# Kernel tuning notes

Measured on AMD Instinct MI355X. Metric: run time of the kernel, lower is better.

The kernel has to match this reference:

```python
import jax, jax.numpy as jnp
from jax import lax
import numpy as np

HEADS = 4
FACTOR = 4
EPS = 1e-12  # torch F.normalize eps


def _to_heads(t):
    # b (head c) (h1 fy) (w1 fx) -> b head (c fx fy) (h1 w1)
    b, C, h, w = t.shape
    c = C // HEADS
    h1, w1 = h // FACTOR, w // FACTOR
    t = t.reshape(b, HEADS, c, h1, FACTOR, w1, FACTOR)       # b,head,c,h1,fy,w1,fx
    t = t.transpose(0, 1, 2, 6, 4, 3, 5)                      # b,head,c,fx,fy,h1,w1
    return t.reshape(b, HEADS, c * FACTOR * FACTOR, h1 * w1)


def _from_heads(t, h, w):
    # b head (c fx fy) (h1 w1) -> b (head c) (h1 fy) (w1 fx)
    b = t.shape[0]
    c = t.shape[2] // (FACTOR * FACTOR)
    h1, w1 = h // FACTOR, w // FACTOR
    t = t.reshape(b, HEADS, c, FACTOR, FACTOR, h1, w1)        # b,head,c,fx,fy,h1,w1
    t = t.transpose(0, 1, 2, 5, 4, 6, 3)                      # b,head,c,h1,fy,w1,fx
    return t.reshape(b, HEADS * c, h, w)


def _l2norm(t):
    n = jnp.sqrt(jnp.sum(t * t, axis=-1, keepdims=True))
    return t / jnp.maximum(n, EPS)


def setup_inputs() -> dict:
    key = jax.random.key(0)
    ks = jax.random.split(key, 4)
    dim = 192
    x = jax.random.normal(ks[0], (8, dim, 128, 128), jnp.float32)
    qkv_w = jax.random.normal(ks[1], (3 * dim, dim), jnp.float32) * 0.05
    qkv_b = jnp.zeros((3 * dim,), jnp.float32)
    dw_w = jax.random.normal(ks[2], (3 * dim, 1, 3, 3), jnp.float32) * 0.05
    dw_b = jnp.zeros((3 * dim,), jnp.float32)
    proj_w = jax.random.normal(ks[3], (dim, dim), jnp.float32) * 0.05
    proj_b = jnp.zeros((dim,), jnp.float32)
    temperature = jnp.ones((HEADS, 1, 1), jnp.float32)
    return dict(x=x, qkv_w=qkv_w, qkv_b=qkv_b, dw_w=dw_w, dw_b=dw_b,
                proj_w=proj_w, proj_b=proj_b, temperature=temperature)


def reference(x, qkv_w, qkv_b, dw_w, dw_b, proj_w, proj_b, temperature):
    b, c, h, w = x.shape
    # 1x1 conv qkv
    qkv = jnp.einsum('bchw,oc->bohw', x, qkv_w) + qkv_b[None, :, None, None]
    # 3x3 depthwise conv (groups = 3*dim)
    qkv = lax.conv_general_dilated(
        qkv, dw_w, window_strides=(1, 1), padding=((1, 1), (1, 1)),
        feature_group_count=3 * c,
        dimension_numbers=('NCHW', 'OIHW', 'NCHW')) + dw_b[None, :, None, None]
    q, k, v = jnp.split(qkv, 3, axis=1)
    # H,W are multiples of FACTOR so the module's pad/unpad is a no-op
    q = _l2norm(_to_heads(q))
    k = _l2norm(_to_heads(k))
    v = _to_heads(v)
    # channel-wise attention: [b,head,d,d] with d = (c/head)*16
    attn = jnp.einsum('bhdn,bhen->bhde', q, k) * temperature[None]
    # softmax_1: exp(x) / (sum exp(x) + 1)
    e = jnp.exp(attn)
    attn = e / (jnp.sum(e, axis=-1, keepdims=True) + 1.0)
    out = jnp.einsum('bhde,bhen->bhdn', attn, v)
    out = _from_heads(out, h, w)
    out = jnp.einsum('bchw,oc->bohw', out, proj_w) + proj_b[None, :, None, None]
    return out
```

## Files before the change

### kernel.cpp

```cpp
#include <hip/hip_runtime.h>

#define HW 16384
#define CDIM 192

typedef short bf16x8 __attribute__((ext_vector_type(8)));
typedef short short8 __attribute__((ext_vector_type(8)));
typedef short short4_t __attribute__((ext_vector_type(4)));
typedef float f32x4  __attribute__((ext_vector_type(4)));

__device__ inline void gload_lds16(const void* g, void* l) {
  __builtin_amdgcn_global_load_lds(
      (const __attribute__((address_space(1))) void*)g,
      (__attribute__((address_space(3))) void*)l, 16, 0, 0);
}

__device__ inline short to_bf16_rne(float f) {
  unsigned u = __float_as_uint(f);
  unsigned r = u + 0x7fffu + ((u >> 16) & 1u);
  return (short)(r >> 16);
}

__device__ inline float b2f(short s) {
  return __uint_as_float(((unsigned)(unsigned short)s) << 16);
}

__device__ inline void split_bf16(float a, short& hi, short& lo) {
  unsigned u = __float_as_uint(a);
  hi = (short)(u >> 16);
  float res = a - __uint_as_float(u & 0xffff0000u);
  lo = (short)(__float_as_uint(res) >> 16);
}

__global__ __launch_bounds__(256) void k_zero(float* __restrict__ p, int n) {
  int i = blockIdx.x * 256 + threadIdx.x;
  if (i < n) p[i] = 0.f;
}

__global__ __launch_bounds__(256) void k_split_w(
    const float* __restrict__ W, short* __restrict__ hi,
    short* __restrict__ lo, int n)
{
  int i = blockIdx.x * 256 + threadIdx.x;
  if (i < n) { short h, l; split_bf16(W[i], h, l); hi[i] = h; lo[i] = l; }
}

#define CMM_LOADB(bv, k0)                                                     \
  { _Pragma("unroll")                                                         \
    for (int kk = 0; kk < 2; ++kk) {                                          \
      const int kcg = kg0 + kk * 2;                                           \
      _Pragma("unroll")                                                       \
      for (int j = 0; j < 8; ++j)                                             \
        bv[kk][j] = xf[(size_t)((k0) + kcg * 8 + j) * HW + n0 + px];          \
    } }

#define CMM_STAGEA1(k0, b)                                                    \
  { _Pragma("unroll")                                                         \
    for (int ii = 0; ii < 3; ++ii) {                                          \
      const int mf = w * 3 + ii;                                   \
      const short* g = Whi + (size_t)(m0 + mf * 16 + lr) * CDIM + (k0) + lq * 8; \
      gload_lds16(g, Ah[b] + mf * 512);                                       \
    } }

#define CMM_WRITEB1(bv, b)                                                    \
  { _Pragma("unroll")                                                         \
    for (int kk = 0; kk < 2; ++kk) {                                          \
      const int kcg = kg0 + kk * 2;                                           \
      short8 s8;                                                              \
      _Pragma("unroll")                                                       \
      for (int j = 0; j < 8; ++j) s8[j] = to_bf16_rne(bv[kk][j]);             \
      *(short8*)&Bh[b][(kcg * 128 + px) * 8] = s8;                            \
    } }

#define CMM_STAGE_PROJ(k0, b)                                                 \
  { _Pragma("unroll")                                                         \
    for (int ii = 0; ii < 6; ++ii) {                                          \
      const int id = w * 6 + ii, arr = id / 12, mf = id % 12;                 \
      const short* Wp = arr ? Wlo : Whi;                                      \
      const short* g = Wp + (size_t)(m0 + mf * 16 + lr) * CDIM + (k0) + lq * 8; \
      gload_lds16(g, (arr ? Al[b] : Ah[b]) + mf * 512);                       \
    }                                                                         \
    _Pragma("unroll")                                                         \
    for (int ii = 0; ii < 4; ++ii) {                                          \
      const int id = w * 4 + ii, arr = id >> 3, sub = id & 7;                 \
      const int kc = sub >> 1, half = sub & 1;                                \
      const short* src = arr ? xl : xh;                                       \
      const short* g = src + ((size_t)((k0) / 8 + kc) * HW + n0 + half * 64 + lane) * 8; \
      gload_lds16(g, (arr ? Bl[b] : Bh[b]) + (kc * 128 + half * 64) * 8);     \
    } }

template <bool SPLITX>
__global__ __launch_bounds__(256) void k_cmm(
    const float* __restrict__ Xf,
    const short* __restrict__ Xhi, const short* __restrict__ Xlo,
    const short* __restrict__ Whi, const short* __restrict__ Wlo,
    const float* __restrict__ bias, void* __restrict__ Outv, int Mtot)
{
  __shared__ short Ah[2][6144], Al[2][6144], Bh[2][4096], Bl[2][4096];
  const int t = threadIdx.x, lane = t & 63, w = t >> 6;
  const int lr = lane & 15, lq = lane >> 4;

  int bb, m0, n0;
  if constexpr (SPLITX) {
    const int flat = blockIdx.x;
    const int g = (flat & 7) * (gridDim.x >> 3) + (flat >> 3);
    bb = g / 384;
    const int rem = g % 384;
    m0 = (rem % 3) * 192;
    n0 = (rem / 3) * 128;
  } else {
    bb = blockIdx.z; m0 = blockIdx.y * 192; n0 = blockIdx.x * 128;
  }

  const float* xf = nullptr;
  const short* xh = nullptr;
  const short* xl = nullptr;
  if constexpr (SPLITX) {
    xf = Xf + (size_t)bb * CDIM * HW;
  } else {
    xh = Xhi + (size_t)bb * 24 * HW * 8;
    xl = Xlo + (size_t)bb * 24 * HW * 8;
  }

  f32x4 acc[3][8] = {};

  if constexpr (SPLITX) {
    const int px = t & 127, kg0 = t >> 7;
    float bv[2][8];
    CMM_LOADB(bv, 0);
    CMM_STAGEA1(0, 0);
    asm volatile("s_waitcnt vmcnt(3)" ::: "memory");
    __builtin_amdgcn_sched_barrier(0);
    CMM_WRITEB1(bv, 0);

    #pragma unroll
    for (int s = 0; s < 6; ++s) {
      const int cur = s & 1;
      asm volatile("s_waitcnt vmcnt(0) lgkmcnt(0)" ::: "memory");
      __builtin_amdgcn_s_barrier();
      __builtin_amdgcn_sched_barrier(0);

      if (s < 5) { CMM_LOADB(bv, (s + 1) << 5); }
      bf16x8 ahf[3];
      #pragma unroll
      for (int mi = 0; mi < 3; ++mi)
        ahf[mi] = *(const bf16x8*)&Ah[cur][(w * 3 + mi) * 512 + lane * 8];
      if (s < 5) { CMM_STAGEA1((s + 1) << 5, cur ^ 1); }
      __builtin_amdgcn_sched_barrier(0);

      __builtin_amdgcn_s_setprio(1);
      #pragma unroll
      for (int j = 0; j < 8; ++j) {
        bf16x8 bsf = *(const bf16x8*)&Bh[cur][(lq * 128 + j * 16 + lr) * 8];
        #pragma unroll
        for (int mi = 0; mi < 3; ++mi)
          acc[mi][j] = __builtin_amdgcn_mfma_f32_16x16x32_bf16(ahf[mi], bsf, acc[mi][j], 0, 0, 0);
      }
      __builtin_amdgcn_s_setprio(0);
      if (s < 5) {
        __builtin_amdgcn_sched_barrier(0);
        asm volatile("s_waitcnt vmcnt(3)" ::: "memory");
        __builtin_amdgcn_sched_barrier(0);
        CMM_WRITEB1(bv, cur ^ 1);
      }
    }
  } else {
    CMM_STAGE_PROJ(0, 0);
    for (int s = 0; s < 6; ++s) {
      const int cur = s & 1;
      asm volatile("s_waitcnt vmcnt(0) lgkmcnt(0)" ::: "memory");
      __builtin_amdgcn_s_barrier();
      __builtin_amdgcn_sched_barrier(0);

      bf16x8 ahf[3], alf[3];
      #pragma unroll
      for (int mi = 0; mi < 3; ++mi) {
        ahf[mi] = *(const bf16x8*)&Ah[cur][(w * 3 + mi) * 512 + lane * 8];
        alf[mi] = *(const bf16x8*)&Al[cur][(w * 3 + mi) * 512 + lane * 8];
      }
      if (s < 5) {
        __builtin_amdgcn_sched_barrier(0);
        CMM_STAGE_PROJ((s + 1) << 5, cur ^ 1);
        __builtin_amdgcn_sched_barrier(0);
      }
      __builtin_amdgcn_s_setprio(1);
      #pragma unroll
      for (int j = 0; j < 8; ++j) {
        bf16x8 bhf = *(const bf16x8*)&Bh[cur][(lq * 128 + j * 16 + lr) * 8];
        bf16x8 blf = *(const bf16x8*)&Bl[cur][(lq * 128 + j * 16 + lr) * 8];
        #pragma unroll
        for (int mi = 0; mi < 3; ++mi) {
          acc[mi][j] = __builtin_amdgcn_mfma_f32_16x16x32_bf16(ahf[mi], bhf, acc[mi][j], 0, 0, 0);
          acc[mi][j] = __builtin_amdgcn_mfma_f32_16x16x32_bf16(ahf[mi], blf, acc[mi][j], 0, 0, 0);
          acc[mi][j] = __builtin_amdgcn_mfma_f32_16x16x32_bf16(alf[mi], bhf, acc[mi][j], 0, 0, 0);
        }
      }
      __builtin_amdgcn_s_setprio(0);
    }
  }

  #pragma unroll
  for (int mi = 0; mi < 3; ++mi) {
    #pragma unroll
    for (int r = 0; r < 4; ++r) {
      const int m = m0 + (w * 3 + mi) * 16 + lq * 4 + r;
      const float bv2 = bias[m];
      const size_t rowo = ((size_t)bb * Mtot + m) * HW + n0;
      #pragma unroll
      for (int j = 0; j < 8; ++j) {
        const int n = j * 16 + lr;
        if constexpr (SPLITX) {
          ((short*)Outv)[rowo + n] = to_bf16_rne(acc[mi][j][r] + bv2);
        } else {
          ((float*)Outv)[rowo + n] = acc[mi][j][r] + bv2;
        }
      }
    }
  }
}

__global__ __launch_bounds__(256) void k_dw(
    const short* __restrict__ tmp,
    const float* __restrict__ dww, const float* __restrict__ dwb,
    short* __restrict__ Qb, short* __restrict__ Kb,
    short* __restrict__ Vt, int b0)
{
  __shared__ short img[16384];
  __shared__ short dwout[16 * 1040];
  __shared__ float sums[16][64];
  __shared__ float rednorm[16];

  const int gc = blockIdx.x, lb = blockIdx.y, b = b0 + lb;
  const int sel = gc / CDIM, chl = gc % CDIM;
  const int head = chl / 48, c = chl % 48;
  const short* gimg = tmp + ((size_t)lb * 576 + gc) * HW;
  const int t = threadIdx.x;

  #pragma unroll
  for (int cch = 0; cch < 8; ++cch)
    gload_lds16(gimg + cch * 2048 + t * 8, img + cch * 2048 + t * 8);

  float wgt[9];
  #pragma unroll
  for (int i = 0; i < 9; ++i) wgt[i] = dww[gc * 9 + i];
  const float bias = dwb[gc];

  asm volatile("s_waitcnt vmcnt(0)" ::: "memory");
  __syncthreads();

  const int fy = (t >> 4) & 3;
  float sqp[4] = {0.f, 0.f, 0.f, 0.f};

  for (int i = 0; i < 8; ++i) {
    const int p8 = i * 2048 + t * 8;
    const int h = p8 >> 7, w0 = p8 & 127;
    float win[3][10];
    #pragma unroll
    for (int dy = 0; dy < 3; ++dy) {
      const int r = h + dy - 1;
      if (r < 0 || r > 127) {
        #pragma unroll
        for (int q = 0; q < 10; ++q) win[dy][q] = 0.f;
      } else {
        const short* rp = img + r * 128 + w0;
        short8 c8 = *(const short8*)rp;
        win[dy][0] = (w0 > 0) ? b2f(rp[-1]) : 0.f;
        #pragma unroll
        for (int q = 0; q < 8; ++q) win[dy][1 + q] = b2f(c8[q]);
        win[dy][9] = (w0 < 120) ? b2f(rp[8]) : 0.f;
      }
    }
    const int na = (h >> 2) * 32 + (w0 >> 2);
    #pragma unroll
    for (int fx = 0; fx < 4; ++fx) {
      float a0 = bias, a1 = bias;
      #pragma unroll
      for (int dy = 0; dy < 3; ++dy)
        #pragma unroll
        for (int dx = 0; dx < 3; ++dx) {
          a0 = fmaf(win[dy][fx + dx], wgt[dy * 3 + dx], a0);
          a1 = fmaf(win[dy][4 + fx + dx], wgt[dy * 3 + dx], a1);
        }
      sqp[fx] = fmaf(a0, a0, sqp[fx]);
      sqp[fx] = fmaf(a1, a1, sqp[fx]);
      *(unsigned*)&dwout[(fx * 4 + fy) * 1040 + na] =
          ((unsigned)(unsigned short)to_bf16_rne(a1) << 16) |
          (unsigned short)to_bf16_rne(a0);
    }
  }

  if (sel < 2) {
    const int slot = (t & 15) | ((t >> 6) << 4);
    #pragma unroll
    for (int fx = 0; fx < 4; ++fx) sums[fx * 4 + fy][slot] = sqp[fx];
    __syncthreads();
    const int row = t >> 4, i16 = t & 15;
    float v = sums[row][i16] + sums[row][i16 + 16] + sums[row][i16 + 32] + sums[row][i16 + 48];
    __syncthreads();
    sums[row][i16] = v;
    __syncthreads();
    if (t < 16) {
      float s = 0.f;
      #pragma unroll
      for (int j = 0; j < 16; ++j) s += sums[t][j];
      rednorm[t] = fmaxf(sqrtf(s), 1e-12f);
    }
  } else {
    __syncthreads();
  }
  __syncthreads();

  if (sel == 2) {
    #pragma unroll
    for (int j = 0; j < 4; ++j) {
      const int n = t + j * 256;
      short8 v0, v1;
      #pragma unroll
      for (int rr = 0; rr < 8; ++rr) v0[rr] = dwout[rr * 1040 + n];
      #pragma unroll
      for (int rr = 0; rr < 8; ++rr) v1[rr] = dwout[(rr + 8) * 1040 + n];
      const size_t o = ((size_t)(b * 4 + head) * 1024 + n) * 768 + c * 16;
      *(short8*)&Vt[o] = v0;
      *(short8*)&Vt[o + 8] = v1;
    }
    return;
  }

  short* dst = (sel == 0) ? Qb : Kb;
  #pragma unroll
  for (int rr = 0; rr < 16; ++rr) {
    const float inv = 1.0f / rednorm[rr];
    const size_t rowoff = ((size_t)(b * 4 + head) * 768 + c * 16 + rr) * 1024;
    #pragma unroll
    for (int j = 0; j < 2; ++j) {
      const int n2 = j * 512 + t * 2;
      const unsigned pk = *(const unsigned*)&dwout[rr * 1040 + n2];
      const float v0 = b2f((short)(pk & 0xffffu)) * inv;
      const float v1 = b2f((short)(pk >> 16)) * inv;
      *(unsigned*)&dst[rowoff + n2] =
          ((unsigned)(unsigned short)to_bf16_rne(v1) << 16) | (unsigned short)to_bf16_rne(v0);
    }
  }
}

__global__ __launch_bounds__(512) void k_qk(
    const short* __restrict__ Qb, const short* __restrict__ Kbf,
    const float* __restrict__ temp,
    short* __restrict__ E, float* __restrict__ Sums)
{
  __shared__ short lds[3][14336];
  const int t = threadIdx.x, lane = t & 63, w = t >> 6;
  const int lr = lane & 15, lq = lane >> 4;

  const int flat = blockIdx.x;
  const int g = (flat & 7) * 48 + (flat >> 3);
  const int bh = g / 12, tile = g % 12;
  const int m0 = (tile / 3) * 192, n0 = (tile % 3) * 256;
  const size_t base = (size_t)bh * 768 * 1024;

  f32x4 acc[6][4] = {};
  const int wm = (w >> 2) * 6, wn = (w & 3) * 4;

  const short* gsrc[4]; size_t goff[4]; int gdst[4]; bool gok[4];
  #pragma unroll
  for (int ii = 0; ii < 4; ++ii) {
    const int id = w * 4 + ii;
    gok[ii] = (id < 28);
    const bool isq = (id < 12);
    gsrc[ii] = isq ? Qb : Kbf;
    const int row = isq ? (m0 + id * 16) : (n0 + (id - 12) * 16);
    goff[ii] = base + (size_t)(row + lr) * 1024 + lq * 8;
    gdst[ii] = (id < 28 ? id : 0) * 512;
  }
  #define QK_STAGE(buf, k0)                                                   \
    { _Pragma("unroll")                                                       \
      for (int ii = 0; ii < 4; ++ii)                                          \
        if (gok[ii]) gload_lds16(gsrc[ii] + goff[ii] + (k0), &lds[buf][gdst[ii]]); }

  QK_STAGE(0, 0);
  QK_STAGE(1, 32);

  for (int step = 0; step < 32; ++step) {
    const int cur = step % 3;
    if (step == 31) { asm volatile("s_waitcnt vmcnt(0)" ::: "memory"); }
    else            { asm volatile("s_waitcnt vmcnt(4)" ::: "memory"); }
    __builtin_amdgcn_s_barrier();
    __builtin_amdgcn_sched_barrier(0);

    bf16x8 ah[6], bf_[4];
    #pragma unroll
    for (int i = 0; i < 6; ++i)
      ah[i] = *(const bf16x8*)&lds[cur][(wm + i) * 512 + lane * 8];
    #pragma unroll
    for (int j = 0; j < 4; ++j)
      bf_[j] = *(const bf16x8*)&lds[cur][(12 + wn + j) * 512 + lane * 8];

    if (step < 30) QK_STAGE((step + 2) % 3, (step + 2) << 5);

    asm volatile("s_waitcnt lgkmcnt(0)" ::: "memory");
    __builtin_amdgcn_sched_barrier(0);
    __builtin_amdgcn_s_setprio(1);
    #pragma unroll
    for (int i = 0; i < 6; ++i)
      #pragma unroll
      for (int j = 0; j < 4; ++j)
        acc[i][j] = __builtin_amdgcn_mfma_f32_16x16x32_bf16(ah[i], bf_[j], acc[i][j], 0, 0, 0);
    __builtin_amdgcn_s_setprio(0);
    __builtin_amdgcn_sched_barrier(0);
  }
  #undef QK_STAGE

  const float tp = temp[bh & 3];
  float* Srow = Sums + bh * 768;
  short* Ep = E + (size_t)bh * 768 * 768;
  #pragma unroll
  for (int i = 0; i < 6; ++i) {
    #pragma unroll
    for (int r = 0; r < 4; ++r) {
      const int m = m0 + (w >> 2) * 96 + i * 16 + lq * 4 + r;
      short* erow = Ep + (size_t)m * 768 + n0 + (w & 3) * 64;
      float rs = 0.f;
      #pragma unroll
      for (int j = 0; j < 4; ++j) {
        const float e = expf(acc[i][j][r] * tp);
        rs += e;
        erow[j * 16 + lr] = to_bf16_rne(e);
      }
      rs += __shfl_xor(rs, 1);
      rs += __shfl_xor(rs, 2);
      rs += __shfl_xor(rs, 4);
      rs += __shfl_xor(rs, 8);
      if (lr == 0) atomicAdd(&Srow[m], rs);
    }
  }
}

__global__ __launch_bounds__(512) void k_av(
    const short* __restrict__ Ebf, const short* __restrict__ Vtb,
    const float* __restrict__ Sums,
    short* __restrict__ Phi, short* __restrict__ Plo)
{
  __shared__ short lds[3][16384];
  const int t = threadIdx.x, lane = t & 63, w = t >> 6;
  const int lr = lane & 15, lq = lane >> 4;

  const int flat = blockIdx.x;
  const int g = (flat & 7) * 48 + (flat >> 3);
  const int bh = g / 12, tile = g % 12;
  const int m0 = (tile / 4) * 256, n0 = (tile % 4) * 256;
  const int head = bh & 3, b = bh >> 2;
  const short* Sp = Ebf + (size_t)bh * 768 * 768;
  const short* Vp = Vtb + (size_t)bh * 1024 * 768;

  f32x4 acc[8][4] = {};
  const int wm = (w >> 2) * 8, wn = (w & 3) * 4;

  const short* gsrc[4]; size_t goff[4]; int gdst[4];
  #pragma unroll
  for (int ii = 0; ii < 4; ++ii) {
    const int id = w * 4 + ii;
    const int arr = id >> 4, s = id & 15;
    gsrc[ii] = arr ? Vp : Sp;
    const int row = (arr ? n0 : m0) + s * 16;
    goff[ii] = (size_t)(row + lr) * 768 + lq * 8;
    gdst[ii] = id * 512;
  }
  #define AV_STAGE(buf, k0)                                                   \
    { _Pragma("unroll")                                                       \
      for (int ii = 0; ii < 4; ++ii)                                          \
        gload_lds16(gsrc[ii] + goff[ii] + (k0), &lds[buf][gdst[ii]]); }

  AV_STAGE(0, 0);
  AV_STAGE(1, 32);

  for (int step = 0; step < 24; ++step) {
    const int cur = step % 3;
    if (step == 23) { asm volatile("s_waitcnt vmcnt(0)" ::: "memory"); }
    else            { asm volatile("s_waitcnt vmcnt(4)" ::: "memory"); }
    __builtin_amdgcn_s_barrier();
    __builtin_amdgcn_sched_barrier(0);

    bf16x8 ea[8], vb[4];
    #pragma unroll
    for (int i = 0; i < 8; ++i)
      ea[i] = *(const bf16x8*)&lds[cur][(wm + i) * 512 + lane * 8];
    #pragma unroll
    for (int j = 0; j < 4; ++j)
      vb[j] = *(const bf16x8*)&lds[cur][(16 + wn + j) * 512 + lane * 8];

    if (step < 22) AV_STAGE((step + 2) % 3, (step + 2) << 5);

    asm volatile("s_waitcnt lgkmcnt(0)" ::: "memory");
    __builtin_amdgcn_sched_barrier(0);
    __builtin_amdgcn_s_setprio(1);
    #pragma unroll
    for (int i = 0; i < 8; ++i)
      #pragma unroll
      for (int j = 0; j < 4; ++j)
        acc[i][j] = __builtin_amdgcn_mfma_f32_16x16x32_bf16(ea[i], vb[j], acc[i][j], 0, 0, 0);
    __builtin_amdgcn_s_setprio(0);
    __builtin_amdgcn_sched_barrier(0);
  }
  #undef AV_STAGE

  const float* Srow = Sums + bh * 768;
  float invv[8][4];
  #pragma unroll
  for (int i = 0; i < 8; ++i)
    #pragma unroll
    for (int r = 0; r < 4; ++r) {
      const int d = m0 + (w >> 2) * 128 + i * 16 + lq * 4 + r;
      invv[i][r] = 1.0f / (Srow[d] + 1.0f);
    }
  #pragma unroll
  for (int i = 0; i < 8; ++i)
    #pragma unroll
    for (int j = 0; j < 4; ++j)
      #pragma unroll
      for (int r = 0; r < 4; ++r)
        acc[i][j][r] *= invv[i][r];

  short* stg = &lds[0][0];
  const int kcp0 = head * 6 + (m0 >> 7);
  const int myc = w >> 2;

  #pragma unroll
  for (int a = 0; a < 2; ++a) {
    #pragma unroll
    for (int c = 0; c < 2; ++c) {
      __syncthreads();
      if (myc == c) {
        #pragma unroll
        for (int j = 0; j < 4; ++j) {
          const int nl = (w & 3) * 64 + j * 16 + lr;
          #pragma unroll
          for (int r = 0; r < 4; ++r) {
            short8 s8;
            #pragma unroll
            for (int i = 0; i < 8; ++i) {
              const float v = acc[i][j][r];
              const unsigned u = __float_as_uint(v);
              if (a == 0) {
                s8[i] = (short)(u >> 16);
              } else {
                const float res = v - __uint_as_float(u & 0xffff0000u);
                s8[i] = (short)(__float_as_uint(res) >> 16);
              }
            }
            const int loff = (((nl >> 5) * 4 + r) * 128 + (nl & 31) * 4 + lq) * 8;
            *(short8*)&stg[loff] = s8;
          }
        }
      }
      __syncthreads();
      short* dst = (a ? Plo : Phi) +
                   ((size_t)(b * 24 + kcp0 + c) * HW + n0 * 16) * 8;
      #pragma unroll
      for (int it = 0; it < 8; ++it) {
        const int idx = it * 4096 + t * 8;
        *(short8*)&dst[idx] = *(const short8*)&stg[idx];
      }
    }
  }
}

extern "C" void kernel_launch(void* const* d_in, const int* in_sizes, int n_in,
                              void* d_out, int out_size, void* d_ws, size_t ws_size,
                              hipStream_t stream) {
  const float* x      = (const float*)d_in[0];
  const float* qkv_w  = (const float*)d_in[1];
  const float* qkv_b  = (const float*)d_in[2];
  const float* dw_w   = (const float*)d_in[3];
  const float* dw_b   = (const float*)d_in[4];
  const float* proj_w = (const float*)d_in[5];
  const float* proj_b = (const float*)d_in[6];
  const float* temp   = (const float*)d_in[7];
  float* out = (float*)d_out;

  float* F = (float*)d_ws;
  const size_t M25 = (size_t)8 * CDIM * HW;
  short* Qb  = (short*)F;
  short* Plo = Qb + M25;
  short* Kb  = (short*)(F + M25);
  short* Vt  = Kb + M25;
  short* Ebf = (short*)(F + 2 * M25);
  short* Phi = Qb;

  short* tmpf = Ebf;
  const size_t ebfBytes  = (size_t)32 * 768 * 768 * 2;
  const size_t baseBytes = 2 * M25 * 4;
  const size_t wsTailBytes = 294912 * 2 + 32 * 768 * 4 + 256;
  int bpi = 2;
  for (int cand = 8; cand >= 2; cand >>= 1) {
    const size_t tmpfBytes = (size_t)cand * 576 * HW * 2;
    const size_t need = baseBytes + (tmpfBytes > ebfBytes ? tmpfBytes : ebfBytes)
                      + wsTailBytes;
    if (ws_size >= need) { bpi = cand; break; }
  }
  const size_t tmpfBytes = (size_t)bpi * 576 * HW * 2;
  short* WS = (short*)((char*)d_ws + baseBytes +
                       (tmpfBytes > ebfBytes ? tmpfBytes : ebfBytes));
  short* Wq_hi = WS;
  short* Wq_lo = WS + 110592;
  short* Wp_hi = WS + 221184;
  short* Wp_lo = WS + 258048;
  float* Sums  = (float*)(WS + 294912);

  k_split_w<<<dim3(432), 256, 0, stream>>>(qkv_w, Wq_hi, Wq_lo, 110592);
  k_split_w<<<dim3(144), 256, 0, stream>>>(proj_w, Wp_hi, Wp_lo, 36864);
  k_zero<<<dim3(96), 256, 0, stream>>>(Sums, 32 * 768);

  for (int b0 = 0; b0 < 8; b0 += bpi) {
    k_cmm<true><<<dim3(384 * bpi), 256, 0, stream>>>(
        x + (size_t)b0 * CDIM * HW, nullptr, nullptr,
        Wq_hi, Wq_lo, qkv_b, tmpf, 576);
    k_dw<<<dim3(576, bpi), 256, 0, stream>>>(
        tmpf, dw_w, dw_b, Qb, Kb, Vt, b0);
  }

  k_qk<<<dim3(384), 512, 0, stream>>>(Qb, Kb, temp, Ebf, Sums);
  k_av<<<dim3(384), 512, 0, stream>>>(Ebf, Vt, Sums, Phi, Plo);
  k_cmm<false><<<dim3(128, 1, 8), 256, 0, stream>>>(
      nullptr, Phi, Plo, Wp_hi, Wp_lo, proj_b, out, 192);
}
```

Before: 540.1 us.

## Widen QKV 1x1-conv GEMM tile to 256 pixels with 8-wave blocks

Splits the templated GEMM into separate QKV and projection kernels and widens the QKV tile from 128 to 256 pixels per block, using 512 threads (8 waves arranged 4x2). The wider tile lets each staged weight fragment serve twice as many pixels, halving weight traffic and block count for the input-projection GEMM. In exchange, LDS use per block rises, only six waves stage weights, and occupancy and wait-count handling change.

```diff
diff --git a/kernel.cpp b/kernel.cpp
--- a/kernel.cpp
+++ b/kernel.cpp
@@ -5,7 +5,6 @@
 
 typedef short bf16x8 __attribute__((ext_vector_type(8)));
 typedef short short8 __attribute__((ext_vector_type(8)));
-typedef short short4_t __attribute__((ext_vector_type(4)));
 typedef float f32x4  __attribute__((ext_vector_type(4)));
 
 __device__ inline void gload_lds16(const void* g, void* l) {
@@ -44,159 +43,177 @@
   if (i < n) { short h, l; split_bf16(W[i], h, l); hi[i] = h; lo[i] = l; }
 }
 
-#define CMM_LOADB(bv, k0)                                                     \
+__global__ __launch_bounds__(512) void k_cmm_qkv(
+    const float* __restrict__ Xf, const short* __restrict__ Whi,
+    const float* __restrict__ bias, short* __restrict__ Out)
+{
+  __shared__ short Ah[2][6144];
+  __shared__ short Bh[2][8192];
+  const int t = threadIdx.x, lane = t & 63, w = t >> 6;
+  const int lr = lane & 15, lq = lane >> 4;
+  const int wrow = w >> 1, wcol = w & 1;
+  const int px = t & 255, kg0 = t >> 8;
+
+  const int flat = blockIdx.x;
+  const int g = (flat & 7) * (gridDim.x >> 3) + (flat >> 3);
+  const int bb = g / 192;
+  const int rem = g % 192;
+  const int m0 = (rem % 3) * 192;
+  const int n0 = (rem / 3) * 256;
+  const float* xf = Xf + (size_t)bb * CDIM * HW;
+
+  f32x4 acc[3][8] = {};
+  float bv[2][8];
+
+#define QKV_LOADB(k0)                                                         \
   { _Pragma("unroll")                                                         \
     for (int kk = 0; kk < 2; ++kk) {                                          \
-      const int kcg = kg0 + kk * 2;                                           \
+      const int kcg = kg0 * 2 + kk;                                           \
       _Pragma("unroll")                                                       \
       for (int j = 0; j < 8; ++j)                                             \
         bv[kk][j] = xf[(size_t)((k0) + kcg * 8 + j) * HW + n0 + px];          \
     } }
 
-#define CMM_STAGEA1(k0, b)                                                    \
-  { _Pragma("unroll")                                                         \
-    for (int ii = 0; ii < 3; ++ii) {                                          \
-      const int mf = w * 3 + ii;                                   \
-      const short* g = Whi + (size_t)(m0 + mf * 16 + lr) * CDIM + (k0) + lq * 8; \
-      gload_lds16(g, Ah[b] + mf * 512);                                       \
+#define QKV_STAGEA(k0, b)                                                     \
+  if (w < 6) {                                                                \
+    _Pragma("unroll")                                                         \
+    for (int ii = 0; ii < 2; ++ii) {                                          \
+      const int mf = w * 2 + ii;                                   \
+      const short* gp = Whi + (size_t)(m0 + mf * 16 + lr) * CDIM + (k0) + lq * 8; \
+      gload_lds16(gp, Ah[b] + mf * 512);                                      \
     } }
 
-#define CMM_WRITEB1(bv, b)                                                    \
+#define QKV_WRITEB(b)                                                         \
   { _Pragma("unroll")                                                         \
     for (int kk = 0; kk < 2; ++kk) {                                          \
-      const int kcg = kg0 + kk * 2;                                           \
+      const int kcg = kg0 * 2 + kk;                                           \
       short8 s8;                                                              \
       _Pragma("unroll")                                                       \
       for (int j = 0; j < 8; ++j) s8[j] = to_bf16_rne(bv[kk][j]);             \
-      *(short8*)&Bh[b][(kcg * 128 + px) * 8] = s8;                            \
+      *(short8*)&Bh[b][(kcg * 256 + px) * 8] = s8;                            \
     } }
 
-#define CMM_STAGE_PROJ(k0, b)                                                 \
+  QKV_LOADB(0);
+  QKV_STAGEA(0, 0);
+  if (w < 6) { asm volatile("s_waitcnt vmcnt(2)" ::: "memory"); }
+  else       { asm volatile("s_waitcnt vmcnt(0)" ::: "memory"); }
+  __builtin_amdgcn_sched_barrier(0);
+  QKV_WRITEB(0);
+
+  #pragma unroll
+  for (int s = 0; s < 6; ++s) {
+    const int cur = s & 1;
+    asm volatile("s_waitcnt vmcnt(0) lgkmcnt(0)" ::: "memory");
+    __builtin_amdgcn_s_barrier();
+    __builtin_amdgcn_sched_barrier(0);
+
+    if (s < 5) { QKV_LOADB((s + 1) << 5); }
+    bf16x8 ahf[3];
+    #pragma unroll
+    for (int mi = 0; mi < 3; ++mi)
+      ahf[mi] = *(const bf16x8*)&Ah[cur][(wrow * 3 + mi) * 512 + lane * 8];
+    if (s < 5) { QKV_STAGEA((s + 1) << 5, cur ^ 1); }
+    __builtin_amdgcn_sched_barrier(0);
+
+    __builtin_amdgcn_s_setprio(1);
+    #pragma unroll
+    for (int j = 0; j < 8; ++j) {
+      bf16x8 bsf = *(const bf16x8*)&Bh[cur][(lq * 256 + wcol * 128 + j * 16 + lr) * 8];
+      #pragma unroll
+      for (int mi = 0; mi < 3; ++mi)
+        acc[mi][j] = __builtin_amdgcn_mfma_f32_16x16x32_bf16(ahf[mi], bsf, acc[mi][j], 0, 0, 0);
+    }
+    __builtin_amdgcn_s_setprio(0);
+    if (s < 5) {
+      __builtin_amdgcn_sched_barrier(0);
+      if (w < 6) { asm volatile("s_waitcnt vmcnt(2)" ::: "memory"); }
+      else       { asm volatile("s_waitcnt vmcnt(0)" ::: "memory"); }
+      __builtin_amdgcn_sched_barrier(0);
+      QKV_WRITEB(cur ^ 1);
+    }
+  }
+#undef QKV_LOADB
+#undef QKV_STAGEA
+#undef QKV_WRITEB
+
+  #pragma unroll
+  for (int mi = 0; mi < 3; ++mi) {
+    #pragma unroll
+    for (int r = 0; r < 4; ++r) {
+      const int m = m0 + (wrow * 3 + mi) * 16 + lq * 4 + r;
+      const float bv2 = bias[m];
+      const size_t rowo = ((size_t)bb * 576 + m) * HW + n0;
+      #pragma unroll
+      for (int j = 0; j < 8; ++j)
+        Out[rowo + wcol * 128 + j * 16 + lr] = to_bf16_rne(acc[mi][j][r] + bv2);
+    }
+  }
+}
+
+__global__ __launch_bounds__(256) void k_cmm_proj(
+    const short* __restrict__ Xhi, const short* __restrict__ Xlo,
+    const short* __restrict__ Whi, const short* __restrict__ Wlo,
+    const float* __restrict__ bias, float* __restrict__ Out, int Mtot)
+{
+  __shared__ short Ah[2][6144], Al[2][6144], Bh[2][4096], Bl[2][4096];
+  const int t = threadIdx.x, lane = t & 63, w = t >> 6;
+  const int lr = lane & 15, lq = lane >> 4;
+  const int bb = blockIdx.z, m0 = blockIdx.y * 192, n0 = blockIdx.x * 128;
+  const short* xh = Xhi + (size_t)bb * 24 * HW * 8;
+  const short* xl = Xlo + (size_t)bb * 24 * HW * 8;
+
+  f32x4 acc[3][8] = {};
+
+#define PROJ_STAGE(k0, b)                                                     \
   { _Pragma("unroll")                                                         \
     for (int ii = 0; ii < 6; ++ii) {                                          \
       const int id = w * 6 + ii, arr = id / 12, mf = id % 12;                 \
       const short* Wp = arr ? Wlo : Whi;                                      \
-      const short* g = Wp + (size_t)(m0 + mf * 16 + lr) * CDIM + (k0) + lq * 8; \
-      gload_lds16(g, (arr ? Al[b] : Ah[b]) + mf * 512);                       \
+      const short* gp = Wp + (size_t)(m0 + mf * 16 + lr) * CDIM + (k0) + lq * 8; \
+      gload_lds16(gp, (arr ? Al[b] : Ah[b]) + mf * 512);                      \
     }                                                                         \
     _Pragma("unroll")                                                         \
     for (int ii = 0; ii < 4; ++ii) {                                          \
       const int id = w * 4 + ii, arr = id >> 3, sub = id & 7;                 \
       const int kc = sub >> 1, half = sub & 1;                                \
       const short* src = arr ? xl : xh;                                       \
-      const short* g = src + ((size_t)((k0) / 8 + kc) * HW + n0 + half * 64 + lane) * 8; \
-      gload_lds16(g, (arr ? Bl[b] : Bh[b]) + (kc * 128 + half * 64) * 8);     \
+      const short* gp = src + ((size_t)((k0) / 8 + kc) * HW + n0 + half * 64 + lane) * 8; \
+      gload_lds16(gp, (arr ? Bl[b] : Bh[b]) + (kc * 128 + half * 64) * 8);    \
     } }
 
-template <bool SPLITX>
-__global__ __launch_bounds__(256) void k_cmm(
-    const float* __restrict__ Xf,
-    const short* __restrict__ Xhi, const short* __restrict__ Xlo,
-    const short* __restrict__ Whi, const short* __restrict__ Wlo,
-    const float* __restrict__ bias, void* __restrict__ Outv, int Mtot)
-{
-  __shared__ short Ah[2][6144], Al[2][6144], Bh[2][4096], Bl[2][4096];
-  const int t = threadIdx.x, lane = t & 63, w = t >> 6;
-  const int lr = lane & 15, lq = lane >> 4;
-
-  int bb, m0, n0;
-  if constexpr (SPLITX) {
-    const int flat = blockIdx.x;
-    const int g = (flat & 7) * (gridDim.x >> 3) + (flat >> 3);
-    bb = g / 384;
-    const int rem = g % 384;
-    m0 = (rem % 3) * 192;
-    n0 = (rem / 3) * 128;
-  } else {
-    bb = blockIdx.z; m0 = blockIdx.y * 192; n0 = blockIdx.x * 128;
-  }
-
-  const float* xf = nullptr;
-  const short* xh = nullptr;
-  const short* xl = nullptr;
-  if constexpr (SPLITX) {
-    xf = Xf + (size_t)bb * CDIM * HW;
-  } else {
-    xh = Xhi + (size_t)bb * 24 * HW * 8;
-    xl = Xlo + (size_t)bb * 24 * HW * 8;
-  }
-
-  f32x4 acc[3][8] = {};
-
-  if constexpr (SPLITX) {
-    const int px = t & 127, kg0 = t >> 7;
-    float bv[2][8];
-    CMM_LOADB(bv, 0);
-    CMM_STAGEA1(0, 0);
-    asm volatile("s_waitcnt vmcnt(3)" ::: "memory");
-    __builtin_amdgcn_sched_barrier(0);
-    CMM_WRITEB1(bv, 0);
-
-    #pragma unroll
-    for (int s = 0; s < 6; ++s) {
-      const int cur = s & 1;
-      asm volatile("s_waitcnt vmcnt(0) lgkmcnt(0)" ::: "memory");
-      __builtin_amdgcn_s_barrier();
+  PROJ_STAGE(0, 0);
+  for (int s = 0; s < 6; ++s) {
+    const int cur = s & 1;
+    asm volatile("s_waitcnt vmcnt(0) lgkmcnt(0)" ::: "memory");
+    __builtin_amdgcn_s_barrier();
+    __builtin_amdgcn_sched_barrier(0);
+
+    bf16x8 ahf[3], alf[3];
+    #pragma unroll
+    for (int mi = 0; mi < 3; ++mi) {
+      ahf[mi] = *(const bf16x8*)&Ah[cur][(w * 3 + mi) * 512 + lane * 8];
+      alf[mi] = *(const bf16x8*)&Al[cur][(w * 3 + mi) * 512 + lane * 8];
+    }
+    if (s < 5) {
       __builtin_amdgcn_sched_barrier(0);
-
-      if (s < 5) { CMM_LOADB(bv, (s + 1) << 5); }
-      bf16x8 ahf[3];
-      #pragma unroll
-      for (int mi = 0; mi < 3; ++mi)
-        ahf[mi] = *(const bf16x8*)&Ah[cur][(w * 3 + mi) * 512 + lane * 8];
-      if (s < 5) { CMM_STAGEA1((s + 1) << 5, cur ^ 1); }
+      PROJ_STAGE((s + 1) << 5, cur ^ 1);
       __builtin_amdgcn_sched_barrier(0);
-
-      __builtin_amdgcn_s_setprio(1);
-      #pragma unroll
-      for (int j = 0; j < 8; ++j) {
-        bf16x8 bsf = *(const bf16x8*)&Bh[cur][(lq * 128 + j * 16 + lr) * 8];
-        #pragma unroll
-        for (int mi = 0; mi < 3; ++mi)
-          acc[mi][j] = __builtin_amdgcn_mfma_f32_16x16x32_bf16(ahf[mi], bsf, acc[mi][j], 0, 0, 0);
+    }
+    __builtin_amdgcn_s_setprio(1);
+    #pragma unroll
+    for (int j = 0; j < 8; ++j) {
+      bf16x8 bhf = *(const bf16x8*)&Bh[cur][(lq * 128 + j * 16 + lr) * 8];
+      bf16x8 blf = *(const bf16x8*)&Bl[cur][(lq * 128 + j * 16 + lr) * 8];
+      #pragma unroll
+      for (int mi = 0; mi < 3; ++mi) {
+        acc[mi][j] = __builtin_amdgcn_mfma_f32_16x16x32_bf16(ahf[mi], bhf, acc[mi][j], 0, 0, 0);
+        acc[mi][j] = __builtin_amdgcn_mfma_f32_16x16x32_bf16(ahf[mi], blf, acc[mi][j], 0, 0, 0);
+        acc[mi][j] = __builtin_amdgcn_mfma_f32_16x16x32_bf16(alf[mi], bhf, acc[mi][j], 0, 0, 0);
       }
-      __builtin_amdgcn_s_setprio(0);
-      if (s < 5) {
-        __builtin_amdgcn_sched_barrier(0);
-        asm volatile("s_waitcnt vmcnt(3)" ::: "memory");
-        __builtin_amdgcn_sched_barrier(0);
-        CMM_WRITEB1(bv, cur ^ 1);
-      }
-    }
-  } else {
-    CMM_STAGE_PROJ(0, 0);
-    for (int s = 0; s < 6; ++s) {
-      const int cur = s & 1;
-      asm volatile("s_waitcnt vmcnt(0) lgkmcnt(0)" ::: "memory");
-      __builtin_amdgcn_s_barrier();
-      __builtin_amdgcn_sched_barrier(0);
-
-      bf16x8 ahf[3], alf[3];
-      #pragma unroll
-      for (int mi = 0; mi < 3; ++mi) {
-        ahf[mi] = *(const bf16x8*)&Ah[cur][(w * 3 + mi) * 512 + lane * 8];
-        alf[mi] = *(const bf16x8*)&Al[cur][(w * 3 + mi) * 512 + lane * 8];
-      }
-      if (s < 5) {
-        __builtin_amdgcn_sched_barrier(0);
-        CMM_STAGE_PROJ((s + 1) << 5, cur ^ 1);
-        __builtin_amdgcn_sched_barrier(0);
-      }
-      __builtin_amdgcn_s_setprio(1);
-      #pragma unroll
-      for (int j = 0; j < 8; ++j) {
-        bf16x8 bhf = *(const bf16x8*)&Bh[cur][(lq * 128 + j * 16 + lr) * 8];
-        bf16x8 blf = *(const bf16x8*)&Bl[cur][(lq * 128 + j * 16 + lr) * 8];
-        #pragma unroll
-        for (int mi = 0; mi < 3; ++mi) {
-          acc[mi][j] = __builtin_amdgcn_mfma_f32_16x16x32_bf16(ahf[mi], bhf, acc[mi][j], 0, 0, 0);
-          acc[mi][j] = __builtin_amdgcn_mfma_f32_16x16x32_bf16(ahf[mi], blf, acc[mi][j], 0, 0, 0);
-          acc[mi][j] = __builtin_amdgcn_mfma_f32_16x16x32_bf16(alf[mi], bhf, acc[mi][j], 0, 0, 0);
-        }
-      }
-      __builtin_amdgcn_s_setprio(0);
-    }
-  }
+    }
+    __builtin_amdgcn_s_setprio(0);
+  }
+#undef PROJ_STAGE
 
   #pragma unroll
   for (int mi = 0; mi < 3; ++mi) {
@@ -206,14 +223,8 @@
       const float bv2 = bias[m];
       const size_t rowo = ((size_t)bb * Mtot + m) * HW + n0;
       #pragma unroll
-      for (int j = 0; j < 8; ++j) {
-        const int n = j * 16 + lr;
-        if constexpr (SPLITX) {
-          ((short*)Outv)[rowo + n] = to_bf16_rne(acc[mi][j][r] + bv2);
-        } else {
-          ((float*)Outv)[rowo + n] = acc[mi][j][r] + bv2;
-        }
-      }
+      for (int j = 0; j < 8; ++j)
+        Out[rowo + j * 16 + lr] = acc[mi][j][r] + bv2;
     }
   }
 }
@@ -610,15 +621,14 @@
   k_zero<<<dim3(96), 256, 0, stream>>>(Sums, 32 * 768);
 
   for (int b0 = 0; b0 < 8; b0 += bpi) {
-    k_cmm<true><<<dim3(384 * bpi), 256, 0, stream>>>(
-        x + (size_t)b0 * CDIM * HW, nullptr, nullptr,
-        Wq_hi, Wq_lo, qkv_b, tmpf, 576);
+    k_cmm_qkv<<<dim3(192 * bpi), 512, 0, stream>>>(
+        x + (size_t)b0 * CDIM * HW, Wq_hi, qkv_b, tmpf);
     k_dw<<<dim3(576, bpi), 256, 0, stream>>>(
         tmpf, dw_w, dw_b, Qb, Kb, Vt, b0);
   }
 
   k_qk<<<dim3(384), 512, 0, stream>>>(Qb, Kb, temp, Ebf, Sums);
   k_av<<<dim3(384), 512, 0, stream>>>(Ebf, Vt, Sums, Phi, Plo);
-  k_cmm<false><<<dim3(128, 1, 8), 256, 0, stream>>>(
-      nullptr, Phi, Plo, Wp_hi, Wp_lo, proj_b, out, 192);
-}
+  k_cmm_proj<<<dim3(128, 1, 8), 256, 0, stream>>>(
+      Phi, Plo, Wp_hi, Wp_lo, proj_b, out, 192);
+}
```

Measured after the change: 533.5 us. About the same (-1.2%).
